# Kernel tuning notes

Measured on AMD Instinct MI355X. Metric: run time of the kernel, lower is better.

The kernel has to match this reference:

```python
import jax, jax.numpy as jnp
import numpy as np

EPS = 1e-5
PI = 3.1415927410125732
B, C, N = 32, 3, 4096


def setup_inputs() -> dict:
    key = jax.random.key(0)
    ks = jax.random.split(key, 16)
    rn = lambda k, shape, scale: (jax.random.normal(k, shape, jnp.float32) * scale)
    z = lambda n: jnp.zeros((n,), jnp.float32)
    o = lambda n: jnp.ones((n,), jnp.float32)
    return {
        "x": jax.random.normal(ks[0], (B, C, N), jnp.float32),
        # conv1x1 weights stored as [out, in] (Conv1d kernel size 1)
        "w1": rn(ks[1], (64, C), 0.5), "b1": z(64), "g1": o(64), "be1": z(64),
        "w2": rn(ks[2], (128, 64), 0.12), "b2": z(128), "g2": o(128), "be2": z(128),
        "w3": rn(ks[3], (1024, 128), 0.09), "b3": z(1024), "g3": o(1024), "be3": z(1024),
        "fw1": rn(ks[4], (512, 1024), 0.03), "fb1": z(512), "g4": o(512), "be4": z(512),
        "fw2": rn(ks[5], (256, 512), 0.044), "fb2": z(256), "g5": o(256), "be5": z(256),
        "fw3": rn(ks[6], (128, 256), 0.0625), "fb3": z(128), "g6": o(128), "be6": z(128),
        "fw4": rn(ks[7], (3, 128), 0.088), "fb4": z(3),
    }


def _bn_cn(h, g, b):
    # BatchNorm1d on [B, C, N]: stats over (batch, spatial), biased variance (train mode)
    m = h.mean((0, 2), keepdims=True)
    v = ((h - m) ** 2).mean((0, 2), keepdims=True)
    return g[None, :, None] * (h - m) * jax.lax.rsqrt(v + EPS) + b[None, :, None]


def _bn_fc(h, g, b):
    # BatchNorm1d on [B, C]: stats over batch
    m = h.mean(0, keepdims=True)
    v = ((h - m) ** 2).mean(0, keepdims=True)
    return g * (h - m) * jax.lax.rsqrt(v + EPS) + b


def _euler_to_rot(ang):
    # ang: [B, 3] = (rx, ry, rz);  R = Rz @ Ry @ Rx per sample
    a, b, c = ang[:, 0], ang[:, 1], ang[:, 2]
    ca, sa = jnp.cos(a), jnp.sin(a)
    cb, sb = jnp.cos(b), jnp.sin(b)
    cc, sc = jnp.cos(c), jnp.sin(c)
    one = jnp.ones_like(a); zero = jnp.zeros_like(a)
    Rx = jnp.stack([jnp.stack([one, zero, zero], -1),
                    jnp.stack([zero, ca, -sa], -1),
                    jnp.stack([zero, sa, ca], -1)], -2)
    Ry = jnp.stack([jnp.stack([cb, zero, sb], -1),
                    jnp.stack([zero, one, zero], -1),
                    jnp.stack([-sb, zero, cb], -1)], -2)
    Rz = jnp.stack([jnp.stack([cc, -sc, zero], -1),
                    jnp.stack([sc, cc, zero], -1),
                    jnp.stack([zero, zero, one], -1)], -2)
    return jnp.matmul(Rz, jnp.matmul(Ry, Rx))  # [B, 3, 3]


def reference(x, w1, b1, g1, be1, w2, b2, g2, be2, w3, b3, g3, be3,
              fw1, fb1, g4, be4, fw2, fb2, g5, be5, fw3, fb3, g6, be6, fw4, fb4):
    h = jax.nn.relu(_bn_cn(jnp.einsum('bcn,oc->bon', x, w1) + b1[None, :, None], g1, be1))
    h = jax.nn.relu(_bn_cn(jnp.einsum('bcn,oc->bon', h, w2) + b2[None, :, None], g2, be2))
    h = jax.nn.relu(_bn_cn(jnp.einsum('bcn,oc->bon', h, w3) + b3[None, :, None], g3, be3))
    h = h.max(axis=2)  # global max pool -> [B, 1024]
    h = jax.nn.relu(_bn_fc(h @ fw1.T + fb1, g4, be4))
    h = jax.nn.relu(_bn_fc(h @ fw2.T + fb2, g5, be5))
    h = jax.nn.relu(_bn_fc(h @ fw3.T + fb3, g6, be6))
    ang = (h @ fw4.T + fb4) * PI  # [B, 3] Euler angles
    return _euler_to_rot(ang)
```

## Files before the change

kernel.cpp:

```cpp
#include <hip/hip_runtime.h>
#include <math.h>


#define EPS 1e-5f
#define PI_F 3.1415927410125732f

typedef unsigned int u32;
typedef unsigned short u16;
typedef __bf16 bf16x8 __attribute__((ext_vector_type(8)));
typedef float f32x4 __attribute__((ext_vector_type(4)));
typedef float f32x16 __attribute__((ext_vector_type(16)));

#define AS1 __attribute__((address_space(1)))
#define AS3 __attribute__((address_space(3)))

__device__ __forceinline__ u16 f2bf(float f) {
  u32 u = __float_as_uint(f);
  return (u16)((u + 0x7FFFu + ((u >> 16) & 1u)) >> 16);
}
__device__ __forceinline__ float bf2f(u16 h) { return __uint_as_float(((u32)h) << 16); }
__device__ __forceinline__ u32 encf(float f) {
  u32 u = __float_as_uint(f);
  return (u & 0x80000000u) ? ~u : (u | 0x80000000u);
}
__device__ __forceinline__ float decf(u32 u) {
  return __uint_as_float((u & 0x80000000u) ? (u ^ 0x80000000u) : ~u);
}

__global__ __launch_bounds__(256) void kA_xpart(const float* __restrict__ x,
    float* __restrict__ xst_part) {
  __shared__ float wsum[4][9];
  int t = threadIdx.x;
  int tg = blockIdx.x * 256 + t;
  int b = tg >> 10, nq = (tg & 1023) << 2;
  const float* xb = x + ((size_t)b * 3) * 4096 + nq;
  float4 a = *(const float4*)(xb);
  float4 c = *(const float4*)(xb + 4096);
  float4 d = *(const float4*)(xb + 8192);
  float p[9];
  p[0] = (a.x + a.y) + (a.z + a.w);
  p[1] = (c.x + c.y) + (c.z + c.w);
  p[2] = (d.x + d.y) + (d.z + d.w);
  p[3] = fmaf(a.x,a.x, fmaf(a.y,a.y, fmaf(a.z,a.z, a.w*a.w)));
  p[4] = fmaf(a.x,c.x, fmaf(a.y,c.y, fmaf(a.z,c.z, a.w*c.w)));
  p[5] = fmaf(a.x,d.x, fmaf(a.y,d.y, fmaf(a.z,d.z, a.w*d.w)));
  p[6] = fmaf(c.x,c.x, fmaf(c.y,c.y, fmaf(c.z,c.z, c.w*c.w)));
  p[7] = fmaf(c.x,d.x, fmaf(c.y,d.y, fmaf(c.z,d.z, c.w*d.w)));
  p[8] = fmaf(d.x,d.x, fmaf(d.y,d.y, fmaf(d.z,d.z, d.w*d.w)));
  #pragma unroll
  for (int k = 0; k < 9; ++k) {
    #pragma unroll
    for (int s = 1; s < 64; s <<= 1) p[k] += __shfl_xor(p[k], s);
  }
  if ((t & 63) == 0) {
    #pragma unroll
    for (int k = 0; k < 9; ++k) wsum[t >> 6][k] = p[k];
  }
  __syncthreads();
  if (t < 9) xst_part[blockIdx.x*9 + t] = wsum[0][t] + wsum[1][t] + wsum[2][t] + wsum[3][t];
}

__global__ __launch_bounds__(256) void kC2_gram(const float* __restrict__ x,
    const float* __restrict__ xst_part,
    const float* __restrict__ w1, const float* __restrict__ b1,
    const float* __restrict__ g1, const float* __restrict__ be1,
    float* __restrict__ gram_part, float* __restrict__ w1f_g, float* __restrict__ b1f_g) {
  __shared__ float xsl[3][1024];
  __shared__ float4 w1s4[64];
  __shared__ __align__(16) char hfrag[4352];
  __shared__ __align__(16) char lfrag[4352];
  __shared__ float mred[256];
  __shared__ float xstL[9];
  int t = threadIdx.x, bi = blockIdx.x;
  int lane = t & 63, wid = t >> 6;
  if (t < 9) { float s = 0.f; for (int p = 0; p < 128; ++p) s += xst_part[p*9 + t]; xstL[t] = s; }
  int b = bi >> 2, n0 = (bi & 3) << 10;
  for (int i = t; i < 3072; i += 256) {
    int c = i >> 10, n = i & 1023;
    xsl[c][n] = x[((size_t)b*3 + c)*4096 + n0 + n];
  }
  __syncthreads();
  if (t < 64) {
    const float inv = 1.f/131072.f;
    float mx = xstL[0]*inv, my = xstL[1]*inv, mz = xstL[2]*inv;
    float cxx = xstL[3]*inv - mx*mx, cxy = xstL[4]*inv - mx*my, cxz = xstL[5]*inv - mx*mz;
    float cyy = xstL[6]*inv - my*my, cyz = xstL[7]*inv - my*mz, czz = xstL[8]*inv - mz*mz;
    float wa = w1[t*3], wb = w1[t*3+1], wc = w1[t*3+2];
    float mu = fmaf(wa, mx, fmaf(wb, my, fmaf(wc, mz, b1[t])));
    float var = wa*wa*cxx + wb*wb*cyy + wc*wc*czz
              + 2.f*(wa*wb*cxy + wa*wc*cxz + wb*wc*cyz);
    float s = g1[t] * rsqrtf(var + EPS);
    float bf = be1[t] + s*(b1[t] - mu);
    w1s4[t] = make_float4(s*wa, s*wb, s*wc, bf);
    if (bi == 0) { w1f_g[t*3] = s*wa; w1f_g[t*3+1] = s*wb; w1f_g[t*3+2] = s*wc; b1f_g[t] = bf; }
  }
  __syncthreads();
  int ch = t & 63, ptg = t >> 6;
  float4 wv = w1s4[ch];
  int wbyte = (ch >> 4)*1088 + (((ch & 15) | (ptg << 4)) << 4);
  const f32x4 zero4 = {0.f,0.f,0.f,0.f};
  f32x4 acc[4] = {zero4, zero4, zero4, zero4};
  float msum = 0.f;
  for (int it = 0; it < 32; ++it) {
    int p0 = (it << 5) | (ptg << 3);
    u32 hw[4], lw[4];
    #pragma unroll
    for (int q = 0; q < 4; ++q) {
      int pA = p0 + 2*q, pB = p0 + 2*q + 1;
      float v0 = fmaxf(fmaf(wv.x, xsl[0][pA], fmaf(wv.y, xsl[1][pA], fmaf(wv.z, xsl[2][pA], wv.w))), 0.f);
      float v1 = fmaxf(fmaf(wv.x, xsl[0][pB], fmaf(wv.y, xsl[1][pB], fmaf(wv.z, xsl[2][pB], wv.w))), 0.f);
      msum += v0 + v1;
      u16 h0 = f2bf(v0), h1 = f2bf(v1);
      hw[q] = (u32)h0 | ((u32)h1 << 16);
      lw[q] = (u32)f2bf(v0 - bf2f(h0)) | ((u32)f2bf(v1 - bf2f(h1)) << 16);
    }
    *(uint4*)(hfrag + wbyte) = make_uint4(hw[0],hw[1],hw[2],hw[3]);
    *(uint4*)(lfrag + wbyte) = make_uint4(lw[0],lw[1],lw[2],lw[3]);
    __syncthreads();
    bf16x8 ah = *(const bf16x8*)(hfrag + wid*1088 + (lane << 4));
    bf16x8 al = *(const bf16x8*)(lfrag + wid*1088 + (lane << 4));
    #pragma unroll
    for (int cg2 = 0; cg2 < 4; ++cg2) {
      bf16x8 bh = *(const bf16x8*)(hfrag + cg2*1088 + (lane << 4));
      bf16x8 bl = *(const bf16x8*)(lfrag + cg2*1088 + (lane << 4));
      acc[cg2] = __builtin_amdgcn_mfma_f32_16x16x32_bf16(al, bh, acc[cg2], 0, 0, 0);
      acc[cg2] = __builtin_amdgcn_mfma_f32_16x16x32_bf16(ah, bl, acc[cg2], 0, 0, 0);
      acc[cg2] = __builtin_amdgcn_mfma_f32_16x16x32_bf16(ah, bh, acc[cg2], 0, 0, 0);
    }
    __syncthreads();
  }
  mred[t] = msum;
  __syncthreads();
  if (t < 64)
    gram_part[(size_t)bi*4160 + 4096 + t] = mred[t] + mred[t+64] + mred[t+128] + mred[t+192];
  #pragma unroll
  for (int cg2 = 0; cg2 < 4; ++cg2) {
    #pragma unroll
    for (int r = 0; r < 4; ++r) {
      int i = (wid << 4) | (((lane >> 4) << 2) | r);
      int j = (cg2 << 4) | (lane & 15);
      gram_part[(size_t)bi*4160 + i*64 + j] = acc[cg2][r];
    }
  }
}

__global__ __launch_bounds__(256) void kR_gramred(const float* __restrict__ gram_part,
    float* __restrict__ gram) {
  int cell = blockIdx.x * 256 + threadIdx.x;
  if (cell >= 4160) return;
  float s = 0.f;
  for (int blk = 0; blk < 128; ++blk) s += gram_part[(size_t)blk*4160 + cell];
  gram[cell] = s;
}

__global__ __launch_bounds__(64) void kD_fold2(const float* __restrict__ gram,
    const float* __restrict__ w2, const float* __restrict__ b2,
    const float* __restrict__ g2, const float* __restrict__ be2,
    float* __restrict__ w2f, float* __restrict__ b2f) {
  __shared__ float wrow[64];
  int o = blockIdx.x, i = threadIdx.x;
  wrow[i] = w2[o*64 + i];
  __syncthreads();
  float si = 0.f;
  #pragma unroll 8
  for (int j = 0; j < 64; ++j) si = fmaf(wrow[j], gram[j*64 + i], si);
  const float inv = 1.f / 131072.f;
  float qi = wrow[i] * si;
  float di = wrow[i] * (gram[4096 + i] * inv);
  #pragma unroll
  for (int d2 = 1; d2 < 64; d2 <<= 1) { qi += __shfl_xor(qi, d2); di += __shfl_xor(di, d2); }
  float mu2 = di + b2[o];
  float var = qi*inv - di*di;
  float s = g2[o] * rsqrtf(var + EPS);
  w2f[o*64 + i] = s * wrow[i];
  if (i == 0) b2f[o] = be2[o] + s*(b2[o] - mu2);
}

__global__ __launch_bounds__(256) void kE2_layer2(const float* __restrict__ x,
    const float* __restrict__ w1f, const float* __restrict__ b1f,
    const float* __restrict__ w2f, const float* __restrict__ b2f,
    u16* __restrict__ h2t_hi, u16* __restrict__ h2t_lo) {
  __shared__ float xs[3][256];
  __shared__ float4 w1s4[64];
  __shared__ __align__(16) char h1h[17408];
  __shared__ __align__(16) char h1l[17408];
  int t = threadIdx.x;
  int b = ((blockIdx.x & 7) << 2) | ((blockIdx.x >> 3) & 3);
  int ntile = (blockIdx.x >> 5) << 8;
  int lane = t & 63, wid = t >> 6;
  int wo = wid & 1, wn = wid >> 1;
  #pragma unroll
  for (int i = 0; i < 3; ++i) {
    int idx = (i << 8) | t;
    int c = idx >> 8, n = idx & 255;
    xs[c][n] = x[((size_t)b*3 + c)*4096 + ntile + n];
  }
  if (t < 64) w1s4[t] = make_float4(w1f[t*3], w1f[t*3+1], w1f[t*3+2], b1f[t]);
  bf16x8 wf_hi[4][2], wf_lo[4][2];
  float4 bvv[4];
  #pragma unroll
  for (int of = 0; of < 4; ++of) {
    int o2r = (wo << 6) | (of << 4) | (lane & 15);
    bvv[of] = *(const float4*)(b2f + (wo << 6) + (of << 4) + ((lane >> 4) << 2));
    #pragma unroll
    for (int ks1 = 0; ks1 < 2; ++ks1) {
      const float* src = w2f + o2r*64 + (ks1 << 5) + ((lane >> 4) << 3);
      float4 f0 = *(const float4*)src;
      float4 f1 = *(const float4*)(src + 4);
      float fv[8] = {f0.x,f0.y,f0.z,f0.w, f1.x,f1.y,f1.z,f1.w};
      u32 hw[4], lw[4];
      #pragma unroll
      for (int p2 = 0; p2 < 4; ++p2) {
        u16 h0 = f2bf(fv[2*p2]), h1 = f2bf(fv[2*p2+1]);
        u16 l0 = f2bf(fv[2*p2] - bf2f(h0)), l1 = f2bf(fv[2*p2+1] - bf2f(h1));
        hw[p2] = (u32)h0 | ((u32)h1 << 16);
        lw[p2] = (u32)l0 | ((u32)l1 << 16);
      }
      uint4 H = make_uint4(hw[0],hw[1],hw[2],hw[3]);
      uint4 L = make_uint4(lw[0],lw[1],lw[2],lw[3]);
      wf_hi[of][ks1] = *(const bf16x8*)&H;
      wf_lo[of][ks1] = *(const bf16x8*)&L;
    }
  }
  __syncthreads();
  const f32x4 zero4 = {0.f,0.f,0.f,0.f};
  for (int chunk = 0; chunk < 2; ++chunk) {
    {
      int n = t >> 1, ks1 = t & 1;
      int nL = (chunk << 7) | n;
      float xa = xs[0][nL], xb = xs[1][nL], xc = xs[2][nL];
      int fb = (((n >> 4) << 1) | ks1) * 1088 + ((n & 15) << 4);
      #pragma unroll
      for (int kq = 0; kq < 4; ++kq) {
        u32 hw[4], lw[4];
        #pragma unroll
        for (int p2 = 0; p2 < 4; ++p2) {
          int k1 = (ks1 << 5) | (kq << 3) | (p2 << 1);
          float4 wv0 = w1s4[k1];
          float4 wv1 = w1s4[k1 + 1];
          float v0 = fmaxf(fmaf(wv0.x, xa, fmaf(wv0.y, xb, fmaf(wv0.z, xc, wv0.w))), 0.f);
          float v1 = fmaxf(fmaf(wv1.x, xa, fmaf(wv1.y, xb, fmaf(wv1.z, xc, wv1.w))), 0.f);
          u16 h0 = f2bf(v0), h1_ = f2bf(v1);
          hw[p2] = (u32)h0 | ((u32)h1_ << 16);
          lw[p2] = (u32)f2bf(v0 - bf2f(h0)) | ((u32)f2bf(v1 - bf2f(h1_)) << 16);
        }
        *(uint4*)(h1h + fb + (kq << 8)) = make_uint4(hw[0],hw[1],hw[2],hw[3]);
        *(uint4*)(h1l + fb + (kq << 8)) = make_uint4(lw[0],lw[1],lw[2],lw[3]);
      }
    }
    __syncthreads();
    #pragma unroll
    for (int nb = 0; nb < 4; ++nb) {
      int fbase = (((wn << 2) | nb) << 1) * 1088 + (lane << 4);
      bf16x8 bh0 = *(const bf16x8*)(h1h + fbase);
      bf16x8 bh1 = *(const bf16x8*)(h1h + fbase + 1088);
      bf16x8 bl0 = *(const bf16x8*)(h1l + fbase);
      bf16x8 bl1 = *(const bf16x8*)(h1l + fbase + 1088);
      int nblk_g = (ntile >> 4) | (chunk << 3) | (wn << 2) | nb;
      #pragma unroll
      for (int of = 0; of < 4; ++of) {
        f32x4 acc;
        acc = __builtin_amdgcn_mfma_f32_16x16x32_bf16(wf_hi[of][0], bl0, zero4, 0, 0, 0);
        acc = __builtin_amdgcn_mfma_f32_16x16x32_bf16(wf_lo[of][0], bh0, acc, 0, 0, 0);
        acc = __builtin_amdgcn_mfma_f32_16x16x32_bf16(wf_hi[of][0], bh0, acc, 0, 0, 0);
        acc = __builtin_amdgcn_mfma_f32_16x16x32_bf16(wf_hi[of][1], bl1, acc, 0, 0, 0);
        acc = __builtin_amdgcn_mfma_f32_16x16x32_bf16(wf_lo[of][1], bh1, acc, 0, 0, 0);
        acc = __builtin_amdgcn_mfma_f32_16x16x32_bf16(wf_hi[of][1], bh1, acc, 0, 0, 0);
        ushort4 hs, ls;
        float v0 = fmaxf(acc[0] + bvv[of].x, 0.f);
        float v1 = fmaxf(acc[1] + bvv[of].y, 0.f);
        float v2 = fmaxf(acc[2] + bvv[of].z, 0.f);
        float v3 = fmaxf(acc[3] + bvv[of].w, 0.f);
        hs.x = f2bf(v0); hs.y = f2bf(v1); hs.z = f2bf(v2); hs.w = f2bf(v3);
        ls.x = f2bf(v0 - bf2f(hs.x)); ls.y = f2bf(v1 - bf2f(hs.y));
        ls.z = f2bf(v2 - bf2f(hs.z)); ls.w = f2bf(v3 - bf2f(hs.w));
        int ks2 = (wo << 1) | (of >> 1);
        int q = ((of & 1) << 1) | ((lane >> 5) & 1);
        int l = (lane & 15) | (q << 4);
        int j0 = ((lane >> 4) & 1) << 2;
        size_t idx = ((((size_t)((b << 8) | nblk_g) << 2) | ks2) << 9) + (l << 3) + j0;
        *(ushort4*)(h2t_hi + idx) = hs;
        *(ushort4*)(h2t_lo + idx) = ls;
      }
    }
    __syncthreads();
  }
}

__global__ __launch_bounds__(256, 3) void k5_layer3(
    const u16* __restrict__ h2t_hi, const u16* __restrict__ h2t_lo,
    const float* __restrict__ w3,
    float* __restrict__ sum3, float* __restrict__ sq3,
    u32* __restrict__ maxe, u32* __restrict__ mine) {
  __shared__ __align__(16) char smem[49152];
  const int t = threadIdx.x, lane = t & 63, wid = t >> 6;
  const int id = blockIdx.x;
  const int xcd = id & 7, rest = id >> 3;
  const int gq = rest & 15, otile = rest >> 4;
  const int g = (gq << 3) | xcd;
  const int b = g >> 2, q = g & 3;

  const size_t gbase = ((size_t)((b << 8) + (q << 6))) << 11;
  auto STAGE = [&](int c, int buf) {
    char* lb = smem + buf * 16384;
    size_t gb = gbase + ((size_t)c << 12);
    #pragma unroll
    for (int i = 0; i < 2; ++i) {
      int off = (i << 12) | (t << 4);
      __builtin_amdgcn_global_load_lds((const AS1 u32*)(h2t_hi + gb + (off >> 1)),
          (AS3 u32*)(lb + off), 16, 0, 0);
    }
    #pragma unroll
    for (int i = 0; i < 2; ++i) {
      int off = (i << 12) | (t << 4);
      __builtin_amdgcn_global_load_lds((const AS1 u32*)(h2t_lo + gb + (off >> 1)),
          (AS3 u32*)(lb + 8192 + off), 16, 0, 0);
    }
  };
  STAGE(0, 0); STAGE(1, 1); STAGE(2, 2);

  bf16x8 wh[8], wl[8];
  {
    int o3 = (otile << 7) | (wid << 5) | (lane & 31);
    #pragma unroll
    for (int ks = 0; ks < 8; ++ks) {
      const float* src = w3 + (size_t)o3*128 + (ks << 4) + ((lane >> 5) << 3);
      float4 f0 = *(const float4*)src;
      float4 f1 = *(const float4*)(src + 4);
      float fv[8] = {f0.x,f0.y,f0.z,f0.w, f1.x,f1.y,f1.z,f1.w};
      u32 hw[4], lw[4];
      #pragma unroll
      for (int p2 = 0; p2 < 4; ++p2) {
        u16 h0 = f2bf(fv[2*p2]), h1 = f2bf(fv[2*p2+1]);
        u16 l0 = f2bf(fv[2*p2] - bf2f(h0)), l1 = f2bf(fv[2*p2+1] - bf2f(h1));
        hw[p2] = (u32)h0 | ((u32)h1 << 16);
        lw[p2] = (u32)l0 | ((u32)l1 << 16);
      }
      uint4 H = make_uint4(hw[0],hw[1],hw[2],hw[3]);
      uint4 L = make_uint4(lw[0],lw[1],lw[2],lw[3]);
      wh[ks] = *(const bf16x8*)&H;
      wl[ks] = *(const bf16x8*)&L;
    }
  }

  const int aoff = (((lane >> 4) & 1) << 12) | ((((lane & 15) | (((lane >> 5) & 1) << 4))) << 4);

  const f32x16 zero16 = {0.f,0.f,0.f,0.f,0.f,0.f,0.f,0.f,0.f,0.f,0.f,0.f,0.f,0.f,0.f,0.f};
  float rs = 0.f, rq = 0.f, rmx = -3.4e38f, rmn = 3.4e38f;

  for (int c = 0; c < 32; ++c) {
    if (c < 30)       asm volatile("s_waitcnt vmcnt(8)" ::: "memory");
    else if (c == 30) asm volatile("s_waitcnt vmcnt(4)" ::: "memory");
    else              asm volatile("s_waitcnt vmcnt(0)" ::: "memory");
    __builtin_amdgcn_s_barrier();
    const char* bp = smem + (c % 3) * 16384;
    const char* bh = bp + aoff;
    const char* bl = bp + 8192 + aoff;
    f32x16 accA, accB, accC;
    __builtin_amdgcn_s_setprio(1);
    #pragma unroll
    for (int ks = 0; ks < 8; ++ks) {
      int ao = ((ks >> 1) << 10) | ((ks & 1) << 9);
      bf16x8 ah = *(const bf16x8*)(bh + ao);
      bf16x8 al = *(const bf16x8*)(bl + ao);
      accA = __builtin_amdgcn_mfma_f32_32x32x16_bf16(al, wh[ks], ks ? accA : zero16, 0, 0, 0);
      accB = __builtin_amdgcn_mfma_f32_32x32x16_bf16(ah, wl[ks], ks ? accB : zero16, 0, 0, 0);
      accC = __builtin_amdgcn_mfma_f32_32x32x16_bf16(ah, wh[ks], ks ? accC : zero16, 0, 0, 0);
    }
    __builtin_amdgcn_s_setprio(0);
    f32x16 acc = (accA + accB) + accC;
    #pragma unroll
    for (int r = 0; r < 16; r += 4) {
      rs += ((acc[r] + acc[r+1]) + (acc[r+2] + acc[r+3]));
      rq = fmaf(acc[r],acc[r], fmaf(acc[r+1],acc[r+1],
           fmaf(acc[r+2],acc[r+2], fmaf(acc[r+3],acc[r+3], rq))));
      rmx = fmaxf(fmaxf(rmx, fmaxf(acc[r],acc[r+1])), fmaxf(acc[r+2],acc[r+3]));
      rmn = fminf(fminf(rmn, fminf(acc[r],acc[r+1])), fminf(acc[r+2],acc[r+3]));
    }
    __builtin_amdgcn_s_barrier();
    if (c < 29) STAGE(c + 3, (c + 3) % 3);
  }

  rs += __shfl_xor(rs, 32);
  rq += __shfl_xor(rq, 32);
  rmx = fmaxf(rmx, __shfl_xor(rmx, 32));
  rmn = fminf(rmn, __shfl_xor(rmn, 32));
  if (lane < 32) {
    int go = (b << 10) | (otile << 7) | (wid << 5) | lane;
    atomicAdd(&sum3[go], rs);
    atomicAdd(&sq3[go], rq);
    atomicMax(&maxe[go], encf(rmx));
    atomicMin(&mine[go], encf(rmn));
  }
}

__global__ void k_fin3_pool(const float* __restrict__ sum3, const float* __restrict__ sq3,
    const u32* __restrict__ maxe, const u32* __restrict__ mine,
    const float* __restrict__ b3,
    const float* __restrict__ g, const float* __restrict__ be, float* __restrict__ pool) {
  int o = blockIdx.x*256 + threadIdx.x;
  float S = 0.f, Q = 0.f;
  for (int b = 0; b < 32; ++b) { S += sum3[(b<<10)|o]; Q += sq3[(b<<10)|o]; }
  const float inv = 1.f/131072.f;
  float ma = S*inv;
  float m = ma + b3[o];
  float var = Q*inv - ma*ma;
  float sc = g[o]*rsqrtf(var + EPS);
  float sh = be[o] - sc*m;
  bool pos = (sc >= 0.f);
  for (int b = 0; b < 32; ++b) {
    float v = decf(pos ? maxe[(b<<10)|o] : mine[(b<<10)|o]) + b3[o];
    pool[(b<<10)|o] = fmaxf(fmaf(sc, v, sh), 0.f);
  }
}

__global__ __launch_bounds__(256) void k_fc_bn_relu(const float* __restrict__ in,
    const float* __restrict__ w, const float* __restrict__ fb,
    const float* __restrict__ g, const float* __restrict__ be,
    float* __restrict__ out, int K, int F) {
  __shared__ float wrow[1024];
  __shared__ float preb[32];
  int o = blockIdx.x, t = threadIdx.x;
  for (int k = t; k < K; k += 256) wrow[k] = w[(size_t)o*K + k];
  __syncthreads();
  int b = t >> 3, j = t & 7;
  int per = K >> 3;
  const float* inb = in + (size_t)b*K + j*per;
  const float* wp  = wrow + j*per;
  float p = 0.f;
  for (int k = 0; k < per; ++k) p = fmaf(inb[k], wp[k], p);
  p += __shfl_xor(p, 1); p += __shfl_xor(p, 2); p += __shfl_xor(p, 4);
  if (j == 0) preb[b] = p + fb[o];
  __syncthreads();
  if (t < 32) {
    float v = preb[t];
    float s = v;
    #pragma unroll
    for (int d = 1; d < 32; d <<= 1) s += __shfl_xor(s, d);
    float m = s * 0.03125f;
    float dv = v - m;
    float q = dv*dv;
    #pragma unroll
    for (int d = 1; d < 32; d <<= 1) q += __shfl_xor(q, d);
    float var = q * 0.03125f;
    float sc = g[o]*rsqrtf(var + EPS);
    out[(size_t)t*F + o] = fmaxf(fmaf(sc, dv, be[o]), 0.f);
  }
}

__global__ __launch_bounds__(128) void k_final(const float* __restrict__ h6,
    const float* __restrict__ fw4, const float* __restrict__ fb4, float* __restrict__ out) {
  __shared__ float angs[32][3];
  int t = threadIdx.x;
  if (t < 96) {
    int b = t / 3, j = t % 3;
    float p = 0.f;
    #pragma unroll 4
    for (int k = 0; k < 128; ++k) p = fmaf(h6[b*128+k], fw4[j*128+k], p);
    angs[b][j] = (p + fb4[j]) * PI_F;
  }
  __syncthreads();
  if (t < 32) {
    float a = angs[t][0], bb = angs[t][1], c = angs[t][2];
    float sa, ca; sincosf(a,  &sa, &ca);
    float sb, cb; sincosf(bb, &sb, &cb);
    float sc, cc; sincosf(c,  &sc, &cc);
    float* o9 = out + t*9;
    o9[0] = cc*cb;
    o9[1] = fmaf(cc*sb, sa, -sc*ca);
    o9[2] = fmaf(cc*sb, ca,  sc*sa);
    o9[3] = sc*cb;
    o9[4] = fmaf(sc*sb, sa,  cc*ca);
    o9[5] = fmaf(sc*sb, ca, -cc*sa);
    o9[6] = -sb;
    o9[7] = cb*sa;
    o9[8] = cb*ca;
  }
}

extern "C" void kernel_launch(void* const* d_in, const int* in_sizes, int n_in,
                              void* d_out, int out_size, void* d_ws, size_t ws_size,
                              hipStream_t stream) {
  (void)in_sizes; (void)n_in; (void)out_size; (void)ws_size;
  const float* x   = (const float*)d_in[0];
  const float* w1  = (const float*)d_in[1];
  const float* b1  = (const float*)d_in[2];
  const float* g1  = (const float*)d_in[3];
  const float* be1 = (const float*)d_in[4];
  const float* w2  = (const float*)d_in[5];
  const float* b2  = (const float*)d_in[6];
  const float* g2  = (const float*)d_in[7];
  const float* be2 = (const float*)d_in[8];
  const float* w3  = (const float*)d_in[9];
  const float* b3  = (const float*)d_in[10];
  const float* g3  = (const float*)d_in[11];
  const float* be3 = (const float*)d_in[12];
  const float* fw1 = (const float*)d_in[13];
  const float* fb1 = (const float*)d_in[14];
  const float* g4  = (const float*)d_in[15];
  const float* be4 = (const float*)d_in[16];
  const float* fw2 = (const float*)d_in[17];
  const float* fb2 = (const float*)d_in[18];
  const float* g5p = (const float*)d_in[19];
  const float* be5 = (const float*)d_in[20];
  const float* fw3 = (const float*)d_in[21];
  const float* fb3 = (const float*)d_in[22];
  const float* g6  = (const float*)d_in[23];
  const float* be6 = (const float*)d_in[24];
  const float* fw4 = (const float*)d_in[25];
  const float* fb4 = (const float*)d_in[26];

  u16* h2t_hi = (u16*)d_ws;
  u16* h2t_lo = (u16*)d_ws + 16777216;
  float* gram_part = (float*)d_ws;
  float* acc0 = (float*)d_ws + 16777216;
  float* xst_part = acc0;
  float* w1f  = acc0 + 1152;
  float* b1f  = acc0 + 1344;
  float* w2f  = acc0 + 1408;
  float* b2f  = acc0 + 9600;
  float* gram = acc0 + 9728;
  float* sum3 = acc0 + 13888;
  float* sq3  = acc0 + 46656;
  u32*   maxe = (u32*)(acc0 + 79424);
  u32*   mine = (u32*)(acc0 + 112192);
  float* pool = acc0 + 144960;
  float* h4v  = acc0 + 177728;
  float* h5v  = acc0 + 194112;
  float* h6v  = acc0 + 202304;

  hipMemsetAsync(acc0 + 13888, 0, 3ull*32768*4, stream);
  hipMemsetAsync(acc0 + 112192, 0xFF, 32768ull*4, stream);

  kA_xpart<<<128, 256, 0, stream>>>(x, xst_part);
  kC2_gram<<<128, 256, 0, stream>>>(x, xst_part, w1, b1, g1, be1, gram_part, w1f, b1f);
  kR_gramred<<<17, 256, 0, stream>>>(gram_part, gram);
  kD_fold2<<<128, 64, 0, stream>>>(gram, w2, b2, g2, be2, w2f, b2f);
  kE2_layer2<<<512, 256, 0, stream>>>(x, w1f, b1f, w2f, b2f, h2t_hi, h2t_lo);
  k5_layer3<<<1024, 256, 0, stream>>>(h2t_hi, h2t_lo, w3, sum3, sq3, maxe, mine);
  k_fin3_pool<<<4, 256, 0, stream>>>(sum3, sq3, maxe, mine, b3, g3, be3, pool);
  k_fc_bn_relu<<<512, 256, 0, stream>>>(pool, fw1, fb1, g4, be4, h4v, 1024, 512);
  k_fc_bn_relu<<<256, 256, 0, stream>>>(h4v, fw2, fb2, g5p, be5, h5v, 512, 256);
  k_fc_bn_relu<<<128, 256, 0, stream>>>(h5v, fw3, fb3, g6, be6, h6v, 256, 128);
  k_final<<<1, 128, 0, stream>>>(h6v, fw4, fb4, (float*)d_out);
}
```

Baseline: 200.4 us.

## Store layer-2 activations as single fp16 and use fp16 MFMA in layer 3

The layer-2 activation tensor is now written once as fp16 instead of as a bf16 hi/lo pair, which halves the intermediate's global traffic and workspace. Layer 3 switches to fp16 MFMAs with the weights split into an fp16 hi/lo pair, so each tile needs two MFMAs instead of three. Each staged chunk now holds two n-fragments and the loop runs 16 iterations instead of 32. The activations lose precision, since a single fp16 is coarser than the bf16 pair, and large values could overflow fp16's range.

```diff
diff --git a/kernel.cpp b/kernel.cpp
--- a/kernel.cpp
+++ b/kernel.cpp
@@ -7,7 +7,9 @@
 
 typedef unsigned int u32;
 typedef unsigned short u16;
+typedef _Float16 f16;
 typedef __bf16 bf16x8 __attribute__((ext_vector_type(8)));
+typedef f16 f16x8 __attribute__((ext_vector_type(8)));
 typedef float f32x4 __attribute__((ext_vector_type(4)));
 typedef float f32x16 __attribute__((ext_vector_type(16)));
 
@@ -19,6 +21,10 @@
   return (u16)((u + 0x7FFFu + ((u >> 16) & 1u)) >> 16);
 }
 __device__ __forceinline__ float bf2f(u16 h) { return __uint_as_float(((u32)h) << 16); }
+__device__ __forceinline__ u16 f2h(float f) {
+  f16 h = (f16)f;
+  union { f16 x; u16 u; } c; c.x = h; return c.u;
+}
 __device__ __forceinline__ u32 encf(float f) {
   u32 u = __float_as_uint(f);
   return (u & 0x80000000u) ? ~u : (u | 0x80000000u);
@@ -179,7 +185,7 @@
 __global__ __launch_bounds__(256) void kE2_layer2(const float* __restrict__ x,
     const float* __restrict__ w1f, const float* __restrict__ b1f,
     const float* __restrict__ w2f, const float* __restrict__ b2f,
-    u16* __restrict__ h2t_hi, u16* __restrict__ h2t_lo) {
+    u16* __restrict__ h2t) {
   __shared__ float xs[3][256];
   __shared__ float4 w1s4[64];
   __shared__ __align__(16) char h1h[17408];
@@ -266,21 +272,17 @@
         acc = __builtin_amdgcn_mfma_f32_16x16x32_bf16(wf_hi[of][1], bl1, acc, 0, 0, 0);
         acc = __builtin_amdgcn_mfma_f32_16x16x32_bf16(wf_lo[of][1], bh1, acc, 0, 0, 0);
         acc = __builtin_amdgcn_mfma_f32_16x16x32_bf16(wf_hi[of][1], bh1, acc, 0, 0, 0);
-        ushort4 hs, ls;
-        float v0 = fmaxf(acc[0] + bvv[of].x, 0.f);
-        float v1 = fmaxf(acc[1] + bvv[of].y, 0.f);
-        float v2 = fmaxf(acc[2] + bvv[of].z, 0.f);
-        float v3 = fmaxf(acc[3] + bvv[of].w, 0.f);
-        hs.x = f2bf(v0); hs.y = f2bf(v1); hs.z = f2bf(v2); hs.w = f2bf(v3);
-        ls.x = f2bf(v0 - bf2f(hs.x)); ls.y = f2bf(v1 - bf2f(hs.y));
-        ls.z = f2bf(v2 - bf2f(hs.z)); ls.w = f2bf(v3 - bf2f(hs.w));
+        ushort4 hs;
+        hs.x = f2h(fmaxf(acc[0] + bvv[of].x, 0.f));
+        hs.y = f2h(fmaxf(acc[1] + bvv[of].y, 0.f));
+        hs.z = f2h(fmaxf(acc[2] + bvv[of].z, 0.f));
+        hs.w = f2h(fmaxf(acc[3] + bvv[of].w, 0.f));
         int ks2 = (wo << 1) | (of >> 1);
         int q = ((of & 1) << 1) | ((lane >> 5) & 1);
         int l = (lane & 15) | (q << 4);
         int j0 = ((lane >> 4) & 1) << 2;
         size_t idx = ((((size_t)((b << 8) | nblk_g) << 2) | ks2) << 9) + (l << 3) + j0;
-        *(ushort4*)(h2t_hi + idx) = hs;
-        *(ushort4*)(h2t_lo + idx) = ls;
+        *(ushort4*)(h2t + idx) = hs;
       }
     }
     __syncthreads();
@@ -288,8 +290,7 @@
 }
 
 __global__ __launch_bounds__(256, 3) void k5_layer3(
-    const u16* __restrict__ h2t_hi, const u16* __restrict__ h2t_lo,
-    const float* __restrict__ w3,
+    const u16* __restrict__ h2t, const float* __restrict__ w3,
     float* __restrict__ sum3, float* __restrict__ sq3,
     u32* __restrict__ maxe, u32* __restrict__ mine) {
   __shared__ __align__(16) char smem[49152];
@@ -300,26 +301,20 @@
   const int g = (gq << 3) | xcd;
   const int b = g >> 2, q = g & 3;
 
-  const size_t gbase = ((size_t)((b << 8) + (q << 6))) << 11;
+  const size_t gbase = ((size_t)b << 19) | ((size_t)q << 17);
   auto STAGE = [&](int c, int buf) {
     char* lb = smem + buf * 16384;
-    size_t gb = gbase + ((size_t)c << 12);
-    #pragma unroll
-    for (int i = 0; i < 2; ++i) {
+    size_t gb = gbase + ((size_t)c << 13);
+    #pragma unroll
+    for (int i = 0; i < 4; ++i) {
       int off = (i << 12) | (t << 4);
-      __builtin_amdgcn_global_load_lds((const AS1 u32*)(h2t_hi + gb + (off >> 1)),
+      __builtin_amdgcn_global_load_lds((const AS1 u32*)(h2t + gb + (off >> 1)),
           (AS3 u32*)(lb + off), 16, 0, 0);
-    }
-    #pragma unroll
-    for (int i = 0; i < 2; ++i) {
-      int off = (i << 12) | (t << 4);
-      __builtin_amdgcn_global_load_lds((const AS1 u32*)(h2t_lo + gb + (off >> 1)),
-          (AS3 u32*)(lb + 8192 + off), 16, 0, 0);
     }
   };
   STAGE(0, 0); STAGE(1, 1); STAGE(2, 2);
 
-  bf16x8 wh[8], wl[8];
+  f16x8 wh[8], wl[8];
   {
     int o3 = (otile << 7) | (wid << 5) | (lane & 31);
     #pragma unroll
@@ -328,18 +323,15 @@
       float4 f0 = *(const float4*)src;
       float4 f1 = *(const float4*)(src + 4);
       float fv[8] = {f0.x,f0.y,f0.z,f0.w, f1.x,f1.y,f1.z,f1.w};
-      u32 hw[4], lw[4];
+      f16x8 vh, vl;
       #pragma unroll
-      for (int p2 = 0; p2 < 4; ++p2) {
-        u16 h0 = f2bf(fv[2*p2]), h1 = f2bf(fv[2*p2+1]);
-        u16 l0 = f2bf(fv[2*p2] - bf2f(h0)), l1 = f2bf(fv[2*p2+1] - bf2f(h1));
-        hw[p2] = (u32)h0 | ((u32)h1 << 16);
-        lw[p2] = (u32)l0 | ((u32)l1 << 16);
+      for (int p2 = 0; p2 < 8; ++p2) {
+        f16 hh = (f16)fv[p2];
+        vh[p2] = hh;
+        vl[p2] = (f16)(fv[p2] - (float)hh);
       }
-      uint4 H = make_uint4(hw[0],hw[1],hw[2],hw[3]);
-      uint4 L = make_uint4(lw[0],lw[1],lw[2],lw[3]);
-      wh[ks] = *(const bf16x8*)&H;
-      wl[ks] = *(const bf16x8*)&L;
+      wh[ks] = vh;
+      wl[ks] = vl;
     }
   }
 
@@ -348,37 +340,37 @@
   const f32x16 zero16 = {0.f,0.f,0.f,0.f,0.f,0.f,0.f,0.f,0.f,0.f,0.f,0.f,0.f,0.f,0.f,0.f};
   float rs = 0.f, rq = 0.f, rmx = -3.4e38f, rmn = 3.4e38f;
 
-  for (int c = 0; c < 32; ++c) {
-    if (c < 30)       asm volatile("s_waitcnt vmcnt(8)" ::: "memory");
-    else if (c == 30) asm volatile("s_waitcnt vmcnt(4)" ::: "memory");
+  for (int c = 0; c < 16; ++c) {
+    if (c < 14)       asm volatile("s_waitcnt vmcnt(8)" ::: "memory");
+    else if (c == 14) asm volatile("s_waitcnt vmcnt(4)" ::: "memory");
     else              asm volatile("s_waitcnt vmcnt(0)" ::: "memory");
     __builtin_amdgcn_s_barrier();
-    const char* bp = smem + (c % 3) * 16384;
-    const char* bh = bp + aoff;
-    const char* bl = bp + 8192 + aoff;
-    f32x16 accA, accB, accC;
+    const char* bp = smem + (c % 3) * 16384 + aoff;
     __builtin_amdgcn_s_setprio(1);
     #pragma unroll
-    for (int ks = 0; ks < 8; ++ks) {
-      int ao = ((ks >> 1) << 10) | ((ks & 1) << 9);
-      bf16x8 ah = *(const bf16x8*)(bh + ao);
-      bf16x8 al = *(const bf16x8*)(bl + ao);
-      accA = __builtin_amdgcn_mfma_f32_32x32x16_bf16(al, wh[ks], ks ? accA : zero16, 0, 0, 0);
-      accB = __builtin_amdgcn_mfma_f32_32x32x16_bf16(ah, wl[ks], ks ? accB : zero16, 0, 0, 0);
-      accC = __builtin_amdgcn_mfma_f32_32x32x16_bf16(ah, wh[ks], ks ? accC : zero16, 0, 0, 0);
+    for (int nf = 0; nf < 2; ++nf) {
+      const char* bn = bp + (nf << 13);
+      f32x16 accA, accB;
+      #pragma unroll
+      for (int ks = 0; ks < 8; ++ks) {
+        int ao = ((ks >> 1) << 10) | ((ks & 1) << 9);
+        f16x8 av = *(const f16x8*)(bn + ao);
+        accA = __builtin_amdgcn_mfma_f32_32x32x16_f16(av, wh[ks], ks ? accA : zero16, 0, 0, 0);
+        accB = __builtin_amdgcn_mfma_f32_32x32x16_f16(av, wl[ks], ks ? accB : zero16, 0, 0, 0);
+      }
+      f32x16 acc = accA + accB;
+      #pragma unroll
+      for (int r = 0; r < 16; r += 4) {
+        rs += ((acc[r] + acc[r+1]) + (acc[r+2] + acc[r+3]));
+        rq = fmaf(acc[r],acc[r], fmaf(acc[r+1],acc[r+1],
+             fmaf(acc[r+2],acc[r+2], fmaf(acc[r+3],acc[r+3], rq))));
+        rmx = fmaxf(fmaxf(rmx, fmaxf(acc[r],acc[r+1])), fmaxf(acc[r+2],acc[r+3]));
+        rmn = fminf(fminf(rmn, fminf(acc[r],acc[r+1])), fminf(acc[r+2],acc[r+3]));
+      }
     }
     __builtin_amdgcn_s_setprio(0);
-    f32x16 acc = (accA + accB) + accC;
-    #pragma unroll
-    for (int r = 0; r < 16; r += 4) {
-      rs += ((acc[r] + acc[r+1]) + (acc[r+2] + acc[r+3]));
-      rq = fmaf(acc[r],acc[r], fmaf(acc[r+1],acc[r+1],
-           fmaf(acc[r+2],acc[r+2], fmaf(acc[r+3],acc[r+3], rq))));
-      rmx = fmaxf(fmaxf(rmx, fmaxf(acc[r],acc[r+1])), fmaxf(acc[r+2],acc[r+3]));
-      rmn = fminf(fminf(rmn, fminf(acc[r],acc[r+1])), fminf(acc[r+2],acc[r+3]));
-    }
     __builtin_amdgcn_s_barrier();
-    if (c < 29) STAGE(c + 3, (c + 3) % 3);
+    if (c < 13) STAGE(c + 3, (c + 3) % 3);
   }
 
   rs += __shfl_xor(rs, 32);
@@ -510,10 +502,9 @@
   const float* fw4 = (const float*)d_in[25];
   const float* fb4 = (const float*)d_in[26];
 
-  u16* h2t_hi = (u16*)d_ws;
-  u16* h2t_lo = (u16*)d_ws + 16777216;
+  u16* h2t = (u16*)d_ws;
   float* gram_part = (float*)d_ws;
-  float* acc0 = (float*)d_ws + 16777216;
+  float* acc0 = (float*)d_ws + 8388608;
   float* xst_part = acc0;
   float* w1f  = acc0 + 1152;
   float* b1f  = acc0 + 1344;
@@ -536,8 +527,8 @@
   kC2_gram<<<128, 256, 0, stream>>>(x, xst_part, w1, b1, g1, be1, gram_part, w1f, b1f);
   kR_gramred<<<17, 256, 0, stream>>>(gram_part, gram);
   kD_fold2<<<128, 64, 0, stream>>>(gram, w2, b2, g2, be2, w2f, b2f);
-  kE2_layer2<<<512, 256, 0, stream>>>(x, w1f, b1f, w2f, b2f, h2t_hi, h2t_lo);
-  k5_layer3<<<1024, 256, 0, stream>>>(h2t_hi, h2t_lo, w3, sum3, sq3, maxe, mine);
+  kE2_layer2<<<512, 256, 0, stream>>>(x, w1f, b1f, w2f, b2f, h2t);
+  k5_layer3<<<1024, 256, 0, stream>>>(h2t, w3, sum3, sq3, maxe, mine);
   k_fin3_pool<<<4, 256, 0, stream>>>(sum3, sq3, maxe, mine, b3, g3, be3, pool);
   k_fc_bn_relu<<<512, 256, 0, stream>>>(pool, fw1, fb1, g4, be4, h4v, 1024, 512);
   k_fc_bn_relu<<<256, 256, 0, stream>>>(h4v, fw2, fb2, g5p, be5, h5v, 512, 256);
```

Result: faster. 171.3 us (-14.5%).
